# Optimization experiments

Measured on AMD Instinct MI355X. Metric: run time of the kernel, lower is better.

Reference implementation:

```python
import jax, jax.numpy as jnp
import numpy as np
import math

B, S, E = 4, 2048, 1024

def setup_inputs() -> dict:
    key = jax.random.key(0)
    ks = jax.random.split(key, 12)
    scale = 1.0 / math.sqrt(E)
    inp = {
        "query": jax.random.normal(ks[0], (B, S, E), jnp.float32),
        "key_": jax.random.normal(ks[1], (B, S, E), jnp.float32),
        "value": jax.random.normal(ks[2], (B, S, E), jnp.float32),
        # causal mask, broadcast over batch: 1 = keep, 0 = mask
        "mask": jnp.broadcast_to(jnp.tril(jnp.ones((S, S), jnp.int32)), (B, S, S)),
        "Wq": jax.random.uniform(ks[3], (E, E), jnp.float32, -scale, scale),
        "bq": jax.random.uniform(ks[4], (E,), jnp.float32, -scale, scale),
        "Wk": jax.random.uniform(ks[5], (E, E), jnp.float32, -scale, scale),
        "bk": jax.random.uniform(ks[6], (E,), jnp.float32, -scale, scale),
        "Wv": jax.random.uniform(ks[7], (E, E), jnp.float32, -scale, scale),
        "bv": jax.random.uniform(ks[8], (E,), jnp.float32, -scale, scale),
        "Wo": jax.random.uniform(ks[9], (E, E), jnp.float32, -scale, scale),
        "bo": jax.random.uniform(ks[10], (E,), jnp.float32, -scale, scale),
    }
    return inp

def reference(query, key_, value, mask, Wq, bq, Wk, bk, Wv, bv, Wo, bo):
    # Linear projections (torch Linear: x @ W.T + b)
    Q = jnp.einsum('bse,fe->bsf', query, Wq) + bq
    K = jnp.einsum('bse,fe->bsf', key_, Wk) + bk
    V = jnp.einsum('bse,fe->bsf', value, Wv) + bv
    # NOTE: module never splits heads; scores over full embed_dim, scaled by sqrt(embed_dim)
    scores = jnp.einsum('bqe,bke->bqk', Q, K) / jnp.sqrt(jnp.asarray(E, Q.dtype))
    scores = jnp.where(mask == 0, -jnp.inf, scores)
    attn = jax.nn.softmax(scores, axis=-1)
    attn_out = jnp.einsum('bqk,bke->bqe', attn, V)
    return jnp.einsum('bse,fe->bsf', attn_out, Wo) + bo
```

## Files before the change

kernel.cpp:

```cpp
#include <hip/hip_runtime.h>

typedef __bf16 bf16;
typedef __attribute__((ext_vector_type(8))) __bf16 bf16x8;
typedef __attribute__((ext_vector_type(4))) __bf16 bf16x4;
typedef __attribute__((ext_vector_type(2))) __bf16 bf16x2;
typedef __attribute__((ext_vector_type(4))) float f32x4;

#define DEVINL __device__ __forceinline__

DEVINL void gload_lds16(const bf16* g, bf16* l) {
    __builtin_amdgcn_global_load_lds(
        (__attribute__((address_space(1))) unsigned int*)(unsigned long long)g,
        (__attribute__((address_space(3))) unsigned int*)l,
        16, 0, 0);
}

DEVINL void xcd_swizzle(int& bx, int& by) {
    const int gx = gridDim.x, gy = gridDim.y;
    const int l = blockIdx.y * gx + blockIdx.x;
    const int xcd = l & 7;
    const int li = l >> 3;
    by = xcd * (gy >> 3) + li / gx;
    bx = li - (li / gx) * gx;
}

__global__ __launch_bounds__(256) void cvt3_f32_to_bf16(
    const float* __restrict__ a, const float* __restrict__ b,
    const float* __restrict__ c, bf16* __restrict__ out, int n4) {
    int i = blockIdx.x * blockDim.x + threadIdx.x;
    if (i >= n4) return;
    const float* src = (blockIdx.z == 0) ? a : (blockIdx.z == 1) ? b : c;
    bf16* dst = out + (size_t)blockIdx.z * (size_t)n4 * 4;
    float4 f = ((const float4*)src)[i];
    bf16x4 o;
    o.x = (bf16)f.x; o.y = (bf16)f.y; o.z = (bf16)f.z; o.w = (bf16)f.w;
    ((bf16x4*)dst)[i] = o;
}

__global__ __launch_bounds__(256) void cvt4_f32_to_bf16(
    const float* __restrict__ a, const float* __restrict__ b,
    const float* __restrict__ c, const float* __restrict__ d,
    bf16* __restrict__ out, int n4) {
    int i = blockIdx.x * blockDim.x + threadIdx.x;
    if (i >= n4) return;
    const float* src = (blockIdx.z == 0) ? a : (blockIdx.z == 1) ? b
                     : (blockIdx.z == 2) ? c : d;
    bf16* dst = out + (size_t)blockIdx.z * (size_t)n4 * 4;
    float4 f = ((const float4*)src)[i];
    bf16x4 o;
    o.x = (bf16)f.x; o.y = (bf16)f.y; o.z = (bf16)f.z; o.w = (bf16)f.w;
    ((bf16x4*)dst)[i] = o;
}

__global__ __launch_bounds__(256) void transpose_bf16(
    const unsigned short* __restrict__ in, unsigned short* __restrict__ out,
    int R, int C) {
    __shared__ unsigned short t[64][65];
    const size_t bo = (size_t)blockIdx.z * R * C;
    const int r0 = blockIdx.y * 64, c0 = blockIdx.x * 64;
#pragma unroll
    for (int i = 0; i < 16; i++) {
        int lin = threadIdx.x + i * 256;
        int r = lin >> 6, c = lin & 63;
        t[r][c] = in[bo + (size_t)(r0 + r) * C + (c0 + c)];
    }
    __syncthreads();
#pragma unroll
    for (int i = 0; i < 16; i++) {
        int lin = threadIdx.x + i * 256;
        int r = lin >> 6, c = lin & 63;
        out[bo + (size_t)(c0 + r) * R + (r0 + c)] = t[c][r];
    }
}

template <int EPI>
__global__ __launch_bounds__(256) void gemm_bt128(
    const bf16* __restrict__ A, const bf16* __restrict__ B,
    const float* __restrict__ bias, void* __restrict__ Cv,
    int M, int N, int K,
    long long sA, long long sB, long long sC, long long sBias,
    float scale) {
    int bx, by;
    xcd_swizzle(bx, by);
    const int bz = blockIdx.z;
    const int m0 = by * 128, n0 = bx * 128;

    A += (size_t)bz * sA;
    B += (size_t)bz * sB;
    if (bias) bias += (size_t)bz * sBias;

    __shared__ __align__(16) bf16 As[128 * 32];
    __shared__ __align__(16) bf16 Bs[128 * 32];

    const int tid = threadIdx.x;
    const int wave = tid >> 6;
    const int lane = tid & 63;
    const int lr = lane & 15;
    const int lq = lane >> 4;
    const int wm = (wave >> 1) * 64;
    const int wn = (wave & 1) * 64;
    const int srow = lane >> 2;
    const int scol = (lane & 3) * 8;

    f32x4 acc[4][4];
    const f32x4 fzero = {0.f, 0.f, 0.f, 0.f};
#pragma unroll
    for (int i = 0; i < 4; i++)
#pragma unroll
        for (int j = 0; j < 4; j++) acc[i][j] = fzero;

    for (int k0 = 0; k0 < K; k0 += 32) {
        const bf16* ga0 = A + (size_t)(m0 + wave * 16 + srow) * K + (k0 + scol);
        const bf16* gb0 = B + (size_t)(n0 + wave * 16 + srow) * K + (k0 + scol);
        gload_lds16(ga0,                  As + wave * 512);
        gload_lds16(ga0 + (size_t)64 * K, As + (wave + 4) * 512);
        gload_lds16(gb0,                  Bs + wave * 512);
        gload_lds16(gb0 + (size_t)64 * K, Bs + (wave + 4) * 512);
        __syncthreads();

        bf16x8 af[4], bfr[4];
#pragma unroll
        for (int i = 0; i < 4; i++)
            af[i] = *(const bf16x8*)(As + (wm + i * 16 + lr) * 32 + lq * 8);
#pragma unroll
        for (int j = 0; j < 4; j++)
            bfr[j] = *(const bf16x8*)(Bs + (wn + j * 16 + lr) * 32 + lq * 8);
#pragma unroll
        for (int i = 0; i < 4; i++)
#pragma unroll
            for (int j = 0; j < 4; j++)
                acc[i][j] = __builtin_amdgcn_mfma_f32_16x16x32_bf16(
                    af[i], bfr[j], acc[i][j], 0, 0, 0);
        __syncthreads();
    }

#pragma unroll
    for (int j = 0; j < 4; j++) {
        const int col = n0 + wn + j * 16 + lr;
        const float bb = bias ? bias[col] : 0.0f;
#pragma unroll
        for (int i = 0; i < 4; i++) {
            const int rowb = m0 + wm + i * 16 + lq * 4;
#pragma unroll
            for (int r = 0; r < 4; r++) {
                if (EPI == 0)
                    ((bf16*)Cv)[(size_t)bz * sC + (size_t)(rowb + r) * N + col] =
                        (bf16)(acc[i][j][r] * scale + bb);
                else
                    ((float*)Cv)[(size_t)bz * sC + (size_t)(rowb + r) * N + col] =
                        acc[i][j][r] * scale + bb;
            }
        }
    }
}

template <int EPI>
__global__ __launch_bounds__(256) void gemm_bt64(
    const bf16* __restrict__ A, const bf16* __restrict__ B,
    const float* __restrict__ bias, void* __restrict__ Cv,
    int M, int N, int K,
    long long sA, long long sB, long long sC, long long sBias,
    float scale, int causal) {
    int bx, by;
    xcd_swizzle(bx, by);
    const int bz = blockIdx.z;
    const int m0 = by * 128, n0 = bx * 64;
    if (causal == 1 && n0 > m0 + 127) return;
    int Keff = K;
    if (causal == 2) { Keff = m0 + 128; if (Keff > K) Keff = K; }

    A += (size_t)bz * sA;
    B += (size_t)bz * sB;
    if (bias) bias += (size_t)bz * sBias;

    __shared__ __align__(16) bf16 As[2][128 * 32];
    __shared__ __align__(16) bf16 Bs[2][64 * 32];

    const int tid = threadIdx.x;
    const int wave = tid >> 6;
    const int lane = tid & 63;
    const int lr = lane & 15;
    const int lq = lane >> 4;
    const int wm = wave * 32;
    const int srow = lane >> 2;
    const int scol = (lane & 3) * 8;

    f32x4 acc[2][4];
    const f32x4 fzero = {0.f, 0.f, 0.f, 0.f};
#pragma unroll
    for (int i = 0; i < 2; i++)
#pragma unroll
        for (int j = 0; j < 4; j++) acc[i][j] = fzero;

    for (int k0 = 0; k0 < Keff; k0 += 64) {
#pragma unroll
        for (int kc = 0; kc < 2; kc++) {
            const bf16* ga0 =
                A + (size_t)(m0 + wave * 16 + srow) * K + (k0 + kc * 32 + scol);
            const bf16* gb0 =
                B + (size_t)(n0 + wave * 16 + srow) * K + (k0 + kc * 32 + scol);
            gload_lds16(ga0,                  As[kc] + wave * 512);
            gload_lds16(ga0 + (size_t)64 * K, As[kc] + (wave + 4) * 512);
            gload_lds16(gb0,                  Bs[kc] + wave * 512);
        }
        __syncthreads();

        bf16x8 af[2][2], bfr[2][4];
#pragma unroll
        for (int kc = 0; kc < 2; kc++) {
#pragma unroll
            for (int i = 0; i < 2; i++)
                af[kc][i] = *(const bf16x8*)(As[kc] + (wm + i * 16 + lr) * 32 + lq * 8);
#pragma unroll
            for (int j = 0; j < 4; j++)
                bfr[kc][j] = *(const bf16x8*)(Bs[kc] + (j * 16 + lr) * 32 + lq * 8);
        }
#pragma unroll
        for (int kc = 0; kc < 2; kc++)
#pragma unroll
            for (int i = 0; i < 2; i++)
#pragma unroll
                for (int j = 0; j < 4; j++)
                    acc[i][j] = __builtin_amdgcn_mfma_f32_16x16x32_bf16(
                        af[kc][i], bfr[kc][j], acc[i][j], 0, 0, 0);
        __syncthreads();
    }

#pragma unroll
    for (int j = 0; j < 4; j++) {
        const int col = n0 + j * 16 + lr;
        const float bb = bias ? bias[col] : 0.0f;
#pragma unroll
        for (int i = 0; i < 2; i++) {
            const int rowb = m0 + wm + i * 16 + lq * 4;
#pragma unroll
            for (int r = 0; r < 4; r++) {
                if (EPI == 0)
                    ((bf16*)Cv)[(size_t)bz * sC + (size_t)(rowb + r) * N + col] =
                        (bf16)(acc[i][j][r] * scale + bb);
                else
                    ((float*)Cv)[(size_t)bz * sC + (size_t)(rowb + r) * N + col] =
                        acc[i][j][r] * scale + bb;
            }
        }
    }
}

__global__ __launch_bounds__(256) void softmax_causal(
    const bf16* __restrict__ Sc, bf16* __restrict__ P, int S) {
    const int row = blockIdx.x;
    const int q = row & (S - 1);
    const bf16* src = Sc + (size_t)row * S;
    bf16* dst = P + (size_t)row * S;
    const int L = q + 1;
    const int tid = threadIdx.x;

    float v[8];
    float mx = -3.0e38f;
#pragma unroll
    for (int i = 0; i < 4; i++) {
        int k = (i * 256 + tid) * 2;
        bf16x2 u = ((const bf16x2*)src)[i * 256 + tid];
        v[2 * i]     = (k < L)     ? (float)u.x : -3.0e38f;
        v[2 * i + 1] = (k + 1 < L) ? (float)u.y : -3.0e38f;
        mx = fmaxf(mx, fmaxf(v[2 * i], v[2 * i + 1]));
    }
#pragma unroll
    for (int off = 32; off > 0; off >>= 1) mx = fmaxf(mx, __shfl_xor(mx, off, 64));
    __shared__ float redm[4], reds[4];
    if ((tid & 63) == 0) redm[tid >> 6] = mx;
    __syncthreads();
    mx = fmaxf(fmaxf(redm[0], redm[1]), fmaxf(redm[2], redm[3]));

    float sum = 0.f;
#pragma unroll
    for (int i = 0; i < 8; i++) {
        float e = (v[i] > -1.0e38f) ? __expf(v[i] - mx) : 0.f;
        v[i] = e;
        sum += e;
    }
#pragma unroll
    for (int off = 32; off > 0; off >>= 1) sum += __shfl_xor(sum, off, 64);
    if ((tid & 63) == 0) reds[tid >> 6] = sum;
    __syncthreads();
    sum = reds[0] + reds[1] + reds[2] + reds[3];
    const float inv = 1.0f / sum;
#pragma unroll
    for (int i = 0; i < 4; i++) {
        bf16x2 o;
        o.x = (bf16)(v[2 * i] * inv);
        o.y = (bf16)(v[2 * i + 1] * inv);
        ((bf16x2*)dst)[i * 256 + tid] = o;
    }
}

extern "C" void kernel_launch(void* const* d_in, const int* in_sizes, int n_in,
                              void* d_out, int out_size, void* d_ws, size_t ws_size,
                              hipStream_t stream) {
    const int B = 4, S = 2048, E = 1024;
    const size_t SBE = (size_t)B * S * E;
    const size_t EE = (size_t)E * E;

    const float* q_in = (const float*)d_in[0];
    const float* k_in = (const float*)d_in[1];
    const float* v_in = (const float*)d_in[2];
    const float* Wq = (const float*)d_in[4];
    const float* bq = (const float*)d_in[5];
    const float* Wk = (const float*)d_in[6];
    const float* bk = (const float*)d_in[7];
    const float* Wv = (const float*)d_in[8];
    const float* bv = (const float*)d_in[9];
    const float* Wo = (const float*)d_in[10];
    const float* bo = (const float*)d_in[11];

    char* ws = (char*)d_ws;
    bf16* qkvb = (bf16*)ws;
    bf16* Sc = (bf16*)ws;
    bf16* AO = (bf16*)ws;
    char* p = ws + (size_t)B * S * S * 4;
    bf16* QKVb = (bf16*)p; p += 3 * SBE * 2;
    bf16* Vt = (bf16*)p; p += SBE * 2;
    bf16* Pb = (bf16*)p; p += (size_t)B * S * S * 2;
    bf16* Wb = (bf16*)p; p += 4 * EE * 2;
    float* biasWS = (float*)p; p += 3 * E * 4;

    bf16* Qb = QKVb;
    bf16* Vb = QKVb + 2 * SBE;
    bf16* Wob = Wb + 3 * EE;

    dim3 gcvt3((int)(SBE / 4 / 256), 1, 3);
    cvt3_f32_to_bf16<<<gcvt3, 256, 0, stream>>>(q_in, k_in, v_in, qkvb, (int)(SBE / 4));
    dim3 gcvt4((int)(EE / 4 / 256), 1, 4);
    cvt4_f32_to_bf16<<<gcvt4, 256, 0, stream>>>(Wq, Wk, Wv, Wo, Wb, (int)(EE / 4));
    hipMemcpyAsync(biasWS,         bq, E * 4, hipMemcpyDeviceToDevice, stream);
    hipMemcpyAsync(biasWS + E,     bk, E * 4, hipMemcpyDeviceToDevice, stream);
    hipMemcpyAsync(biasWS + 2 * E, bv, E * 4, hipMemcpyDeviceToDevice, stream);

    dim3 blk(256);
    dim3 gproj(E / 128, (B * S) / 128, 3);
    gemm_bt128<0><<<gproj, blk, 0, stream>>>(qkvb, Wb, biasWS, QKVb,
                                             B * S, E, E,
                                             (long long)SBE, (long long)EE,
                                             (long long)SBE, (long long)E, 1.f);

    dim3 gt(E / 64, S / 64, B);
    transpose_bf16<<<gt, blk, 0, stream>>>((const unsigned short*)Vb,
                                           (unsigned short*)Vt, S, E);

    dim3 gsc(S / 64, S / 128, B);
    gemm_bt64<0><<<gsc, blk, 0, stream>>>(Qb, QKVb + SBE, nullptr, Sc, S, S, E,
                                          (long long)S * E, (long long)S * E,
                                          (long long)S * S, 0, 0.03125f, 1);

    softmax_causal<<<B * S, 256, 0, stream>>>(Sc, Pb, S);

    dim3 gpv(E / 64, S / 128, B);
    gemm_bt64<0><<<gpv, blk, 0, stream>>>(Pb, Vt, nullptr, AO, S, E, S,
                                          (long long)S * S, (long long)E * S,
                                          (long long)S * E, 0, 1.f, 2);

    dim3 gout(E / 64, (B * S) / 128, 1);
    gemm_bt64<1><<<gout, blk, 0, stream>>>(AO, Wob, bo, (float*)d_out,
                                           B * S, E, E, 0, 0, 0, 0, 1.f, 0);
}
```

Before: 421.7 us.

## Double-buffer GEMM LDS tiles with XOR swizzle and pass biases directly

Both GEMM kernels now prefetch the next K-slice into a second LDS buffer while computing on the current one, needing only one barrier per iteration. The LDS layout is XOR-swizzled on both the global-to-LDS write and the fragment reads to reduce bank conflicts. The three bias memcpys before the projection GEMM are removed; the kernel selects bq/bk/bv by blockIdx.z instead. The extra LDS buffer in gemm_bt128 doubles its shared memory, which may lower occupancy.

```diff
diff --git a/kernel.cpp b/kernel.cpp
--- a/kernel.cpp
+++ b/kernel.cpp
@@ -23,6 +23,7 @@
     by = xcd * (gy >> 3) + li / gx;
     bx = li - (li / gx) * gx;
 }
+
 
 __global__ __launch_bounds__(256) void cvt3_f32_to_bf16(
     const float* __restrict__ a, const float* __restrict__ b,
@@ -76,9 +77,10 @@
 template <int EPI>
 __global__ __launch_bounds__(256) void gemm_bt128(
     const bf16* __restrict__ A, const bf16* __restrict__ B,
-    const float* __restrict__ bias, void* __restrict__ Cv,
+    const float* __restrict__ bias0, const float* __restrict__ bias1,
+    const float* __restrict__ bias2, void* __restrict__ Cv,
     int M, int N, int K,
-    long long sA, long long sB, long long sC, long long sBias,
+    long long sA, long long sB, long long sC,
     float scale) {
     int bx, by;
     xcd_swizzle(bx, by);
@@ -87,10 +89,10 @@
 
     A += (size_t)bz * sA;
     B += (size_t)bz * sB;
-    if (bias) bias += (size_t)bz * sBias;
-
-    __shared__ __align__(16) bf16 As[128 * 32];
-    __shared__ __align__(16) bf16 Bs[128 * 32];
+    const float* bias = (bz == 0) ? bias0 : (bz == 1) ? bias1 : bias2;
+
+    __shared__ __align__(16) bf16 As[2][128 * 32];
+    __shared__ __align__(16) bf16 Bs[2][128 * 32];
 
     const int tid = threadIdx.x;
     const int wave = tid >> 6;
@@ -100,7 +102,12 @@
     const int wm = (wave >> 1) * 64;
     const int wn = (wave & 1) * 64;
     const int srow = lane >> 2;
-    const int scol = (lane & 3) * 8;
+    const int scol = ((lane & 3) ^ ((lane >> 3) & 3)) * 8;
+
+    const bf16* gA = A + (size_t)(m0 + wave * 16 + srow) * K + scol;
+    const bf16* gB = B + (size_t)(n0 + wave * 16 + srow) * K + scol;
+    const size_t rowskip = (size_t)64 * K;
+    const int rsw = (lq ^ ((lr >> 1) & 3)) * 8;
 
     f32x4 acc[4][4];
     const f32x4 fzero = {0.f, 0.f, 0.f, 0.f};
@@ -109,30 +116,37 @@
 #pragma unroll
         for (int j = 0; j < 4; j++) acc[i][j] = fzero;
 
+#define STAGE128(bufi)                                        \
+    do {                                                      \
+        gload_lds16(gA,           As[bufi] + wave * 512);     \
+        gload_lds16(gA + rowskip, As[bufi] + (wave + 4) * 512); \
+        gload_lds16(gB,           Bs[bufi] + wave * 512);     \
+        gload_lds16(gB + rowskip, Bs[bufi] + (wave + 4) * 512); \
+        gA += 32; gB += 32;                                   \
+    } while (0)
+
+    STAGE128(0);
+    int cur = 0;
     for (int k0 = 0; k0 < K; k0 += 32) {
-        const bf16* ga0 = A + (size_t)(m0 + wave * 16 + srow) * K + (k0 + scol);
-        const bf16* gb0 = B + (size_t)(n0 + wave * 16 + srow) * K + (k0 + scol);
-        gload_lds16(ga0,                  As + wave * 512);
-        gload_lds16(ga0 + (size_t)64 * K, As + (wave + 4) * 512);
-        gload_lds16(gb0,                  Bs + wave * 512);
-        gload_lds16(gb0 + (size_t)64 * K, Bs + (wave + 4) * 512);
         __syncthreads();
+        if (k0 + 32 < K) STAGE128(cur ^ 1);
 
         bf16x8 af[4], bfr[4];
 #pragma unroll
         for (int i = 0; i < 4; i++)
-            af[i] = *(const bf16x8*)(As + (wm + i * 16 + lr) * 32 + lq * 8);
+            af[i] = *(const bf16x8*)(As[cur] + (wm + i * 16 + lr) * 32 + rsw);
 #pragma unroll
         for (int j = 0; j < 4; j++)
-            bfr[j] = *(const bf16x8*)(Bs + (wn + j * 16 + lr) * 32 + lq * 8);
+            bfr[j] = *(const bf16x8*)(Bs[cur] + (wn + j * 16 + lr) * 32 + rsw);
 #pragma unroll
         for (int i = 0; i < 4; i++)
 #pragma unroll
             for (int j = 0; j < 4; j++)
                 acc[i][j] = __builtin_amdgcn_mfma_f32_16x16x32_bf16(
                     af[i], bfr[j], acc[i][j], 0, 0, 0);
-        __syncthreads();
-    }
+        cur ^= 1;
+    }
+#undef STAGE128
 
 #pragma unroll
     for (int j = 0; j < 4; j++) {
@@ -159,7 +173,7 @@
     const bf16* __restrict__ A, const bf16* __restrict__ B,
     const float* __restrict__ bias, void* __restrict__ Cv,
     int M, int N, int K,
-    long long sA, long long sB, long long sC, long long sBias,
+    long long sA, long long sB, long long sC,
     float scale, int causal) {
     int bx, by;
     xcd_swizzle(bx, by);
@@ -171,7 +185,6 @@
 
     A += (size_t)bz * sA;
     B += (size_t)bz * sB;
-    if (bias) bias += (size_t)bz * sBias;
 
     __shared__ __align__(16) bf16 As[2][128 * 32];
     __shared__ __align__(16) bf16 Bs[2][64 * 32];
@@ -183,7 +196,12 @@
     const int lq = lane >> 4;
     const int wm = wave * 32;
     const int srow = lane >> 2;
-    const int scol = (lane & 3) * 8;
+    const int scol = ((lane & 3) ^ ((lane >> 3) & 3)) * 8;
+
+    const bf16* gA = A + (size_t)(m0 + wave * 16 + srow) * K + scol;
+    const bf16* gB = B + (size_t)(n0 + wave * 16 + srow) * K + scol;
+    const size_t rowskip = (size_t)64 * K;
+    const int rsw = (lq ^ ((lr >> 1) & 3)) * 8;
 
     f32x4 acc[2][4];
     const f32x4 fzero = {0.f, 0.f, 0.f, 0.f};
@@ -192,39 +210,36 @@
 #pragma unroll
         for (int j = 0; j < 4; j++) acc[i][j] = fzero;
 
-    for (int k0 = 0; k0 < Keff; k0 += 64) {
-#pragma unroll
-        for (int kc = 0; kc < 2; kc++) {
-            const bf16* ga0 =
-                A + (size_t)(m0 + wave * 16 + srow) * K + (k0 + kc * 32 + scol);
-            const bf16* gb0 =
-                B + (size_t)(n0 + wave * 16 + srow) * K + (k0 + kc * 32 + scol);
-            gload_lds16(ga0,                  As[kc] + wave * 512);
-            gload_lds16(ga0 + (size_t)64 * K, As[kc] + (wave + 4) * 512);
-            gload_lds16(gb0,                  Bs[kc] + wave * 512);
-        }
+#define STAGE64(bufi)                                          \
+    do {                                                       \
+        gload_lds16(gA,           As[bufi] + wave * 512);      \
+        gload_lds16(gA + rowskip, As[bufi] + (wave + 4) * 512); \
+        gload_lds16(gB,           Bs[bufi] + wave * 512);      \
+        gA += 32; gB += 32;                                    \
+    } while (0)
+
+    STAGE64(0);
+    int cur = 0;
+    for (int k0 = 0; k0 < Keff; k0 += 32) {
         __syncthreads();
-
-        bf16x8 af[2][2], bfr[2][4];
-#pragma unroll
-        for (int kc = 0; kc < 2; kc++) {
-#pragma unroll
-            for (int i = 0; i < 2; i++)
-                af[kc][i] = *(const bf16x8*)(As[kc] + (wm + i * 16 + lr) * 32 + lq * 8);
+        if (k0 + 32 < Keff) STAGE64(cur ^ 1);
+
+        bf16x8 af[2], bfr[4];
+#pragma unroll
+        for (int i = 0; i < 2; i++)
+            af[i] = *(const bf16x8*)(As[cur] + (wm + i * 16 + lr) * 32 + rsw);
+#pragma unroll
+        for (int j = 0; j < 4; j++)
+            bfr[j] = *(const bf16x8*)(Bs[cur] + (j * 16 + lr) * 32 + rsw);
+#pragma unroll
+        for (int i = 0; i < 2; i++)
 #pragma unroll
             for (int j = 0; j < 4; j++)
-                bfr[kc][j] = *(const bf16x8*)(Bs[kc] + (j * 16 + lr) * 32 + lq * 8);
-        }
-#pragma unroll
-        for (int kc = 0; kc < 2; kc++)
-#pragma unroll
-            for (int i = 0; i < 2; i++)
-#pragma unroll
-                for (int j = 0; j < 4; j++)
-                    acc[i][j] = __builtin_amdgcn_mfma_f32_16x16x32_bf16(
-                        af[kc][i], bfr[kc][j], acc[i][j], 0, 0, 0);
-        __syncthreads();
-    }
+                acc[i][j] = __builtin_amdgcn_mfma_f32_16x16x32_bf16(
+                    af[i], bfr[j], acc[i][j], 0, 0, 0);
+        cur ^= 1;
+    }
+#undef STAGE64
 
 #pragma unroll
     for (int j = 0; j < 4; j++) {
@@ -322,7 +337,6 @@
     bf16* Vt = (bf16*)p; p += SBE * 2;
     bf16* Pb = (bf16*)p; p += (size_t)B * S * S * 2;
     bf16* Wb = (bf16*)p; p += 4 * EE * 2;
-    float* biasWS = (float*)p; p += 3 * E * 4;
 
     bf16* Qb = QKVb;
     bf16* Vb = QKVb + 2 * SBE;
@@ -332,16 +346,13 @@
     cvt3_f32_to_bf16<<<gcvt3, 256, 0, stream>>>(q_in, k_in, v_in, qkvb, (int)(SBE / 4));
     dim3 gcvt4((int)(EE / 4 / 256), 1, 4);
     cvt4_f32_to_bf16<<<gcvt4, 256, 0, stream>>>(Wq, Wk, Wv, Wo, Wb, (int)(EE / 4));
-    hipMemcpyAsync(biasWS,         bq, E * 4, hipMemcpyDeviceToDevice, stream);
-    hipMemcpyAsync(biasWS + E,     bk, E * 4, hipMemcpyDeviceToDevice, stream);
-    hipMemcpyAsync(biasWS + 2 * E, bv, E * 4, hipMemcpyDeviceToDevice, stream);
 
     dim3 blk(256);
     dim3 gproj(E / 128, (B * S) / 128, 3);
-    gemm_bt128<0><<<gproj, blk, 0, stream>>>(qkvb, Wb, biasWS, QKVb,
+    gemm_bt128<0><<<gproj, blk, 0, stream>>>(qkvb, Wb, bq, bk, bv, QKVb,
                                              B * S, E, E,
                                              (long long)SBE, (long long)EE,
-                                             (long long)SBE, (long long)E, 1.f);
+                                             (long long)SBE, 1.f);
 
     dim3 gt(E / 64, S / 64, B);
     transpose_bf16<<<gt, blk, 0, stream>>>((const unsigned short*)Vb,
@@ -350,16 +361,16 @@
     dim3 gsc(S / 64, S / 128, B);
     gemm_bt64<0><<<gsc, blk, 0, stream>>>(Qb, QKVb + SBE, nullptr, Sc, S, S, E,
                                           (long long)S * E, (long long)S * E,
-                                          (long long)S * S, 0, 0.03125f, 1);
+                                          (long long)S * S, 0.03125f, 1);
 
     softmax_causal<<<B * S, 256, 0, stream>>>(Sc, Pb, S);
 
     dim3 gpv(E / 64, S / 128, B);
     gemm_bt64<0><<<gpv, blk, 0, stream>>>(Pb, Vt, nullptr, AO, S, E, S,
                                           (long long)S * S, (long long)E * S,
-                                          (long long)S * E, 0, 1.f, 2);
+                                          (long long)S * E, 1.f, 2);
 
     dim3 gout(E / 64, (B * S) / 128, 1);
     gemm_bt64<1><<<gout, blk, 0, stream>>>(AO, Wob, bo, (float*)d_out,
-                                           B * S, E, E, 0, 0, 0, 0, 1.f, 0);
-}
+                                           B * S, E, E, 0, 0, 0, 1.f, 0);
+}
```

Result: no change. 419.3 us (-0.6%).
